# Optimization experiments

Measured on AMD Instinct MI355X. Metric: run time of the kernel, lower is better.

The kernel has to match this reference:

```python
import jax, jax.numpy as jnp
import numpy as np
from jax import lax

B, C, H, W = 4, 128, 128, 128
DG = 2          # deformable groups
K = 9           # 3x3 kernel
EPS = 1e-5


def conv2d(x, w, stride=1, pad=1):
    return lax.conv_general_dilated(
        x, w, (stride, stride), [(pad, pad), (pad, pad)],
        dimension_numbers=("NCHW", "OIHW", "NCHW"))


def bn(x, p):
    # p: [4, C] = gamma, beta, running_mean, running_var (eval-mode BN)
    g, b, m, v = p[0], p[1], p[2], p[3]
    inv = g / jnp.sqrt(v + EPS)
    return x * inv[:, None, None] + (b - m * inv)[:, None, None]


def deform_sample(x, py, px):
    # x: [B,C,H,W]; py/px: [B,DG,K,H,W] absolute sample coords
    Bb, Cc, Hh, Ww = x.shape
    Cg = Cc // DG
    xg = x.reshape(Bb, DG, Cg, Hh * Ww)
    y0 = jnp.floor(py); x0 = jnp.floor(px)
    fy = py - y0; fx = px - x0
    y0i = y0.astype(jnp.int32); x0i = x0.astype(jnp.int32)

    def corner(yi, xi, wgt):
        valid = (yi >= 0) & (yi < Hh) & (xi >= 0) & (xi < Ww)
        idx = (jnp.clip(yi, 0, Hh - 1) * Ww + jnp.clip(xi, 0, Ww - 1)).reshape(Bb, DG, -1)
        v = jnp.take_along_axis(xg, idx[:, :, None, :], axis=3)  # [B,DG,Cg,K*H*W]
        return v * (wgt * valid).reshape(Bb, DG, 1, -1)

    val = (corner(y0i, x0i, (1 - fy) * (1 - fx))
           + corner(y0i, x0i + 1, (1 - fy) * fx)
           + corner(y0i + 1, x0i, fy * (1 - fx))
           + corner(y0i + 1, x0i + 1, fy * fx))
    return val.reshape(Bb, DG, Cg, K, Hh, Ww)


def modulated_deform_conv(x, off_w, off_b, dc_w, dc_b):
    Bb, Cc, Hh, Ww = x.shape
    off_out = conv2d(x, off_w) + off_b[None, :, None, None]   # [B,3*DG*K,H,W]
    o = off_out[:, :2 * DG * K].reshape(Bb, DG, K, 2, Hh, Ww)
    mask = jax.nn.sigmoid(off_out[:, 2 * DG * K:]).reshape(Bb, DG, K, Hh, Ww)
    ky = (jnp.arange(K) // 3 - 1).astype(x.dtype)
    kx = (jnp.arange(K) % 3 - 1).astype(x.dtype)
    iy = jnp.arange(Hh, dtype=x.dtype)[:, None]
    ix = jnp.arange(Ww, dtype=x.dtype)[None, :]
    py = o[:, :, :, 0] + iy + ky[None, None, :, None, None]
    px = o[:, :, :, 1] + ix + kx[None, None, :, None, None]
    g = deform_sample(x, py, px) * mask[:, :, None]            # [B,DG,Cg,K,H,W]
    wr = dc_w.reshape(dc_w.shape[0], DG, Cc // DG, K)          # [O,DG,Cg,K]
    out = jnp.einsum("odck,bdckhw->bohw", wr, g)
    return out + dc_b[None, :, None, None]


def setup_inputs() -> dict:
    key = jax.random.key(0)
    ks = jax.random.split(key, 16)
    s3 = 1.0 / np.sqrt(C * 9)
    s1 = 1.0 / np.sqrt(C)

    def bn_params(k):
        k1, k2, k3, k4 = jax.random.split(k, 4)
        return jnp.stack([
            jax.random.uniform(k1, (C,)) + 0.5,
            jax.random.normal(k2, (C,)) * 0.1,
            jax.random.normal(k3, (C,)) * 0.1,
            jax.random.uniform(k4, (C,)) + 0.5])

    return {
        "x": jax.random.normal(ks[0], (B, C, H, W), jnp.float32),
        "rb_w1": jax.random.normal(ks[1], (C, C, 3, 3), jnp.float32) * s3,
        "rb_b1": jax.random.normal(ks[2], (C,), jnp.float32) * 0.01,
        "rb_bn1": bn_params(ks[3]),
        "rb_w2": jax.random.normal(ks[4], (C, C, 3, 3), jnp.float32) * s3,
        "rb_b2": jax.random.normal(ks[5], (C,), jnp.float32) * 0.01,
        "rb_bn2": bn_params(ks[6]),
        "off_w": jax.random.normal(ks[7], (3 * DG * K, C, 3, 3), jnp.float32) * s3 * 0.1,
        "off_b": jax.random.normal(ks[8], (3 * DG * K,), jnp.float32) * 0.01,
        "dc_w": jax.random.normal(ks[9], (C, C, 3, 3), jnp.float32) * s3,
        "dc_b": jax.random.normal(ks[10], (C,), jnp.float32) * 0.01,
        "bn1": bn_params(ks[11]),
        "cv2_w": jax.random.normal(ks[12], (C, C, 1, 1), jnp.float32) * s1,
        "bn2": bn_params(ks[13]),
    }


def reference(x, rb_w1, rb_b1, rb_bn1, rb_w2, rb_b2, rb_bn2,
              off_w, off_b, dc_w, dc_b, bn1, cv2_w, bn2):
    # ResBlock (stride=1, n_in==n_out -> identity shortcut)
    h = jax.nn.relu(bn(conv2d(x, rb_w1) + rb_b1[None, :, None, None], rb_bn1))
    h = bn(conv2d(h, rb_w2) + rb_b2[None, :, None, None], rb_bn2)
    h = jax.nn.relu(h + x)
    # modulated deformable conv + BN + LeakyReLU(0.1)
    h = modulated_deform_conv(h, off_w, off_b, dc_w, dc_b)
    h = jax.nn.leaky_relu(bn(h, bn1), 0.1)
    # 1x1 conv (no bias) + BN + LeakyReLU(0.1)
    h = jax.nn.leaky_relu(bn(conv2d(h, cv2_w, pad=0), bn2), 0.1)
    # residual (downsample is None: in==out, stride==1)
    return x + h
```

## Files before the change

### kernel.cpp

```cpp
#include <hip/hip_runtime.h>
#include <math.h>

#define BB 4
#define EPSV 1e-5f

typedef __attribute__((ext_vector_type(8))) short short8;
typedef __attribute__((ext_vector_type(4))) float floatx4;
typedef __attribute__((ext_vector_type(4))) int intx4;
typedef __attribute__((ext_vector_type(4))) unsigned short ushort4v;

__device__ inline float b2f(unsigned short u) {
    unsigned v = ((unsigned)u) << 16;
    return __builtin_bit_cast(float, v);
}
__device__ inline unsigned short f2b(float f) {
    unsigned u = __builtin_bit_cast(unsigned, f);
    u += 0x7FFFu + ((u >> 16) & 1u);
    return (unsigned short)(u >> 16);
}
__device__ inline unsigned short f2b_fast(float f) {
    unsigned u = __builtin_bit_cast(unsigned, f);
    return (unsigned short)((u + 0x8000u) >> 16);
}

__global__ __launch_bounds__(256) void transpose_k(const float* __restrict__ x,
                                                   unsigned short* __restrict__ xb) {
    __shared__ unsigned short t[64][136];
    const int tid = threadIdx.x;
    const int px0 = blockIdx.x * 64;
    const int b = blockIdx.y;
    const int pxr = tid & 63;
    const int c0 = tid >> 6;
#pragma unroll
    for (int i = 0; i < 32; ++i) {
        int c = c0 + i * 4;
        float v = x[(((size_t)b * 128 + c) << 14) + px0 + pxr];
        t[pxr][c] = f2b(v);
    }
    __syncthreads();
#pragma unroll
    for (int i = 0; i < 4; ++i) {
        int idx = tid + i * 256;
        int px = idx >> 4;
        int c8 = idx & 15;
        short8 v = *(const short8*)&t[px][c8 * 8];
        *(short8*)&xb[(((size_t)b << 14) + px0 + px) * 128 + c8 * 8] = v;
    }
}

template<int MPAD, int OCH>
__global__ __launch_bounds__(256) void repack_conv_frag(const float* __restrict__ w,
                                                        unsigned short* __restrict__ dst) {
    int t = blockIdx.x * 256 + threadIdx.x;
    if (t >= 1152 * MPAD) return;
    const int NMT2 = MPAD / 16;
    int j = t & 7, lane = (t >> 3) & 63, rest = t >> 9;
    int mt = rest % NMT2, step = rest / NMT2;
    int oc = mt * 16 + (lane & 15);
    int k = step * 32 + ((lane >> 4) << 3) + j;
    int half = k / 576;
    int tap = (k - half * 576) >> 6;
    int c = half * 64 + (k & 63);
    float v = (oc < OCH) ? w[((size_t)oc * 128 + c) * 9 + tap] : 0.f;
    dst[t] = f2b(v);
}

__global__ __launch_bounds__(256) void repack_dc_frag(const float* __restrict__ w,
                                                      unsigned short* __restrict__ dst) {
    int t = blockIdx.x * 256 + threadIdx.x;
    if (t >= 1152 * 128) return;
    int j = t & 7, lane = (t >> 3) & 63, rest = t >> 9;
    int mt = rest & 7, step = rest >> 3;
    int oc = mt * 16 + (lane & 15);
    int k = step * 32 + ((lane >> 4) << 3) + j;
    int dk = k >> 6, c = k & 63;
    int d = (dk >= 9) ? 1 : 0;
    int kk = dk - d * 9;
    float v = w[((size_t)oc * 128 + d * 64 + c) * 9 + kk];
    dst[t] = f2b(v);
}

__global__ __launch_bounds__(256) void repack_cv2_frag(const float* __restrict__ w,
                                                       unsigned short* __restrict__ dst) {
    int t = blockIdx.x * 256 + threadIdx.x;
    if (t >= 128 * 128) return;
    int j = t & 7, lane = (t >> 3) & 63, rest = t >> 9;
    int mt = rest & 7, step = rest >> 3;
    int oc = mt * 16 + (lane & 15);
    int k = step * 32 + ((lane >> 4) << 3) + j;
    dst[t] = f2b(w[oc * 128 + k]);
}

template<int NMT, int MODE>
__global__ __launch_bounds__(256, 2) void conv3x3_mfma(
    const unsigned short* __restrict__ in, const unsigned short* __restrict__ wf,
    const float* __restrict__ bias, const float* __restrict__ bnp,
    const float* __restrict__ res, void* __restrict__ outv)
{
    __shared__ unsigned short sm[3][130][72];
    const int tid = threadIdx.x;
    const int lane = tid & 63, wid = tid >> 6;
    const int wm = wid & 1, wn = wid >> 1;
    const int h = blockIdx.x;
    const int b = blockIdx.y;
    const int n16 = lane & 15, quad = lane >> 4;

    short8 L[13];

    auto stage_load = [&](int half) {
#pragma unroll
        for (int rnd = 0; rnd < 13; ++rnd) {
            int idx = rnd * 256 + tid;
            short8 v = {0, 0, 0, 0, 0, 0, 0, 0};
            if (idx < 3120) {
                int c8 = idx & 7;
                int wl = (idx >> 3) % 130;
                int r  = (idx >> 3) / 130;
                int hh = h - 1 + r, ww = wl - 1;
                if ((unsigned)hh < 128u && (unsigned)ww < 128u)
                    v = *(const short8*)&in[(((size_t)b << 14) + hh * 128 + ww) * 128 + half * 64 + c8 * 8];
            }
            L[rnd] = v;
        }
    };
    auto stage_write = [&]() {
#pragma unroll
        for (int rnd = 0; rnd < 13; ++rnd) {
            int idx = rnd * 256 + tid;
            if (idx < 3120) {
                int c8 = idx & 7;
                int wl = (idx >> 3) % 130;
                int r  = (idx >> 3) / 130;
                *(short8*)&sm[r][wl][c8 * 8] = L[rnd];
            }
        }
    };

    floatx4 acc[NMT][4];
#pragma unroll
    for (int mt = 0; mt < NMT; ++mt)
#pragma unroll
        for (int nt = 0; nt < 4; ++nt)
            acc[mt][nt] = (floatx4){0.f, 0.f, 0.f, 0.f};

    auto compute = [&](int half) {
#pragma unroll
        for (int tap = 0; tap < 9; ++tap) {
            const int ky = tap / 3, kx = tap % 3;
#pragma unroll
            for (int cc = 0; cc < 2; ++cc) {
                const int step = half * 18 + tap * 2 + cc;
                short8 a[NMT], bf[4];
#pragma unroll
                for (int nt = 0; nt < 4; ++nt)
                    bf[nt] = *(const short8*)&sm[ky][wn * 64 + nt * 16 + n16 + kx][cc * 32 + quad * 8];
#pragma unroll
                for (int mt = 0; mt < NMT; ++mt)
                    a[mt] = *(const short8*)&wf[((size_t)(step * (2 * NMT) + wm * NMT + mt) * 64 + lane) * 8];
#pragma unroll
                for (int mt = 0; mt < NMT; ++mt)
#pragma unroll
                    for (int nt = 0; nt < 4; ++nt)
                        acc[mt][nt] = __builtin_amdgcn_mfma_f32_16x16x32_bf16(a[mt], bf[nt], acc[mt][nt], 0, 0, 0);
            }
        }
    };

    stage_load(0);
    stage_write();
    __syncthreads();
    stage_load(1);
    compute(0);
    __syncthreads();
    stage_write();
    __syncthreads();
    compute(1);

#pragma unroll
    for (int mt = 0; mt < NMT; ++mt) {
        const int ocb = (wm * NMT + mt) * 16 + quad * 4;
        float Ae[4], Be[4];
#pragma unroll
        for (int r = 0; r < 4; ++r) {
            int oc = ocb + r;
            if (MODE == 0) {
                Ae[r] = 1.f;
                Be[r] = (oc < 54) ? bias[oc] : 0.f;
            } else {
                float g = bnp[oc], be = bnp[128 + oc], m = bnp[256 + oc], vv = bnp[384 + oc];
                float inv = g * rsqrtf(vv + EPSV);
                Ae[r] = inv;
                Be[r] = be - m * inv + bias[oc] * inv;
            }
        }
#pragma unroll
        for (int nt = 0; nt < 4; ++nt) {
            int pxg = h * 128 + wn * 64 + nt * 16 + n16;
            if (MODE == 0) {
                float* outf = (float*)outv;
#pragma unroll
                for (int r = 0; r < 4; ++r) {
                    int oc = ocb + r;
                    if (oc < 54)
                        outf[(((size_t)(b * 54 + oc)) << 14) + pxg] = acc[mt][nt][r] + Be[r];
                }
            } else {
                ushort4v pk;
#pragma unroll
                for (int r = 0; r < 4; ++r) {
                    float v = acc[mt][nt][r] * Ae[r] + Be[r];
                    if (MODE == 2) v += res[(((size_t)b * 128 + ocb + r) << 14) + pxg];
                    v = fmaxf(v, 0.f);
                    pk[r] = f2b(v);
                }
                *(ushort4v*)&((unsigned short*)outv)[((size_t)((b << 14) + pxg)) * 128 + ocb] = pk;
            }
        }
    }
}

__global__ __launch_bounds__(256, 4) void deform_mfma(
    const unsigned short* __restrict__ src, const float* __restrict__ off,
    const unsigned short* __restrict__ wf, const float* __restrict__ dcb,
    const float* __restrict__ bnp, unsigned short* __restrict__ out)
{
    __shared__ unsigned short gt[2][64][72];
    __shared__ floatx4 smw[3][64];
    __shared__ intx4   sma[3][64];
    const int tid = threadIdx.x;
    const int lane = tid & 63, wid = tid >> 6;
    const int wm = wid & 1, wn = wid >> 1;
    const int w0 = (blockIdx.x & 1) * 64;
    const int h = blockIdx.x >> 1;
    const int b = blockIdx.y;
    const int n16 = lane & 15, quad = lane >> 4;
    const int q = tid & 7;
    const int pxq = tid >> 3 & 31;

    const char* srcbyte = (const char*)src + ((size_t)b << 22);
    const float* offpx = off + (((size_t)(b * 54)) << 14) + h * 128 + w0 + tid;

    auto math = [&](int dk, int slot) {
        float oy = offpx[(size_t)(2 * dk) << 14];
        float ox = offpx[(size_t)(2 * dk + 1) << 14];
        float mz = offpx[(size_t)(36 + dk) << 14];
        int d = (dk >= 9) ? 1 : 0;
        int kk = dk - d * 9;
        float ms = 1.f / (1.f + __expf(-mz));
        float py = oy + (float)h + (float)(kk / 3 - 1);
        float pxs = ox + (float)(w0 + tid) + (float)(kk % 3 - 1);
        float y0f = floorf(py), x0f = floorf(pxs);
        float fy = py - y0f, fx = pxs - x0f;
        int y0 = (int)y0f, x0 = (int)x0f;
        int y1 = y0 + 1, x1 = x0 + 1;
        float w00 = (1.f - fy) * (1.f - fx) * ms, w01 = (1.f - fy) * fx * ms;
        float w10 = fy * (1.f - fx) * ms, w11 = fy * fx * ms;
        if ((unsigned)y0 >= 128u) { w00 = 0.f; w01 = 0.f; }
        if ((unsigned)y1 >= 128u) { w10 = 0.f; w11 = 0.f; }
        if ((unsigned)x0 >= 128u) { w00 = 0.f; w10 = 0.f; }
        if ((unsigned)x1 >= 128u) { w01 = 0.f; w11 = 0.f; }
        int y0c = min(max(y0, 0), 127), y1c = min(max(y1, 0), 127);
        int x0c = min(max(x0, 0), 127), x1c = min(max(x1, 0), 127);
        int chb = d * 128;
        smw[slot][tid] = (floatx4){w00, w01, w10, w11};
        sma[slot][tid] = (intx4){((y0c * 128 + x0c) << 8) + chb, ((y0c * 128 + x1c) << 8) + chb,
                                 ((y1c * 128 + x0c) << 8) + chb, ((y1c * 128 + x1c) << 8) + chb};
    };

    floatx4 wA[2];
    short8 g[2][4];
    auto gather = [&](int slot) {
#pragma unroll
        for (int ph = 0; ph < 2; ++ph) {
            int pxl = ph * 32 + pxq;
            floatx4 wv = smw[slot][pxl];
            intx4 av = sma[slot][pxl];
            wA[ph] = wv;
#pragma unroll
            for (int c = 0; c < 4; ++c)
                g[ph][c] = *(const short8*)(srcbyte + (size_t)(av[c] + q * 16));
        }
    };

    floatx4 acc[4][2];
#pragma unroll
    for (int mt = 0; mt < 4; ++mt)
#pragma unroll
        for (int nt = 0; nt < 2; ++nt)
            acc[mt][nt] = (floatx4){0.f, 0.f, 0.f, 0.f};

    if (tid < 64) { math(0, 0); math(1, 1); }
    __syncthreads();
    gather(0);

    int buf = 0;
    for (int dk = 0; dk < 18; ++dk) {
#pragma unroll
        for (int ph = 0; ph < 2; ++ph) {
            short8 o8;
#pragma unroll
            for (int j = 0; j < 8; ++j) {
                float v = wA[ph][0] * b2f((unsigned short)g[ph][0][j])
                        + wA[ph][1] * b2f((unsigned short)g[ph][1][j])
                        + wA[ph][2] * b2f((unsigned short)g[ph][2][j])
                        + wA[ph][3] * b2f((unsigned short)g[ph][3][j]);
                o8[j] = (short)f2b_fast(v);
            }
            *(short8*)&gt[buf][ph * 32 + pxq][q * 8] = o8;
        }
        if (tid < 64 && dk < 16) math(dk + 2, (dk + 2) % 3);
        __syncthreads();
        if (dk < 17) gather((dk + 1) % 3);

#pragma unroll
        for (int hf = 0; hf < 2; ++hf) {
            int s = dk * 2 + hf;
            short8 a[4], bfr[2];
#pragma unroll
            for (int nt = 0; nt < 2; ++nt)
                bfr[nt] = *(const short8*)&gt[buf][wn * 32 + nt * 16 + n16][hf * 32 + quad * 8];
#pragma unroll
            for (int mt = 0; mt < 4; ++mt)
                a[mt] = *(const short8*)&wf[((size_t)(s * 8 + wm * 4 + mt) * 64 + lane) * 8];
#pragma unroll
            for (int mt = 0; mt < 4; ++mt)
#pragma unroll
                for (int nt = 0; nt < 2; ++nt)
                    acc[mt][nt] = __builtin_amdgcn_mfma_f32_16x16x32_bf16(a[mt], bfr[nt], acc[mt][nt], 0, 0, 0);
        }
        buf ^= 1;
    }

#pragma unroll
    for (int mt = 0; mt < 4; ++mt) {
        const int ocb = (wm * 4 + mt) * 16 + quad * 4;
        float Ae[4], Be[4];
#pragma unroll
        for (int r = 0; r < 4; ++r) {
            int oc = ocb + r;
            float gg = bnp[oc], be = bnp[128 + oc], m = bnp[256 + oc], vv = bnp[384 + oc];
            float inv = gg * rsqrtf(vv + EPSV);
            Ae[r] = inv;
            Be[r] = be - m * inv + dcb[oc] * inv;
        }
#pragma unroll
        for (int nt = 0; nt < 2; ++nt) {
            int pxg2 = h * 128 + w0 + wn * 32 + nt * 16 + n16;
            ushort4v pk;
#pragma unroll
            for (int r = 0; r < 4; ++r) {
                float v = acc[mt][nt][r] * Ae[r] + Be[r];
                v = (v > 0.f) ? v : 0.1f * v;
                pk[r] = f2b(v);
            }
            *(ushort4v*)&out[((size_t)((b << 14) + pxg2)) * 128 + ocb] = pk;
        }
    }
}

__global__ __launch_bounds__(256, 4) void conv1x1_mfma(
    const unsigned short* __restrict__ in, const unsigned short* __restrict__ wf,
    const float* __restrict__ bnp, const float* __restrict__ x, float* __restrict__ out)
{
    const int tid = threadIdx.x;
    const int lane = tid & 63, wid = tid >> 6;
    const int wm = wid & 1, wn = wid >> 1;
    const int w0 = (blockIdx.x & 1) * 64;
    const int h = blockIdx.x >> 1;
    const int b = blockIdx.y;
    const int n16 = lane & 15, quad = lane >> 4;

    floatx4 acc[4][2];
#pragma unroll
    for (int mt = 0; mt < 4; ++mt)
#pragma unroll
        for (int nt = 0; nt < 2; ++nt)
            acc[mt][nt] = (floatx4){0.f, 0.f, 0.f, 0.f};

#pragma unroll
    for (int s = 0; s < 4; ++s) {
        short8 a[4], bfr[2];
#pragma unroll
        for (int nt = 0; nt < 2; ++nt) {
            int px = h * 128 + w0 + wn * 32 + nt * 16 + n16;
            bfr[nt] = *(const short8*)&in[((size_t)((b << 14) + px)) * 128 + s * 32 + quad * 8];
        }
#pragma unroll
        for (int mt = 0; mt < 4; ++mt)
            a[mt] = *(const short8*)&wf[((size_t)(s * 8 + wm * 4 + mt) * 64 + lane) * 8];
#pragma unroll
        for (int mt = 0; mt < 4; ++mt)
#pragma unroll
            for (int nt = 0; nt < 2; ++nt)
                acc[mt][nt] = __builtin_amdgcn_mfma_f32_16x16x32_bf16(a[mt], bfr[nt], acc[mt][nt], 0, 0, 0);
    }

#pragma unroll
    for (int mt = 0; mt < 4; ++mt) {
        const int ocb = (wm * 4 + mt) * 16 + quad * 4;
        float Ae[4], Be[4];
#pragma unroll
        for (int r = 0; r < 4; ++r) {
            int oc = ocb + r;
            float g = bnp[oc], be = bnp[128 + oc], m = bnp[256 + oc], vv = bnp[384 + oc];
            float inv = g * rsqrtf(vv + EPSV);
            Ae[r] = inv;
            Be[r] = be - m * inv;
        }
#pragma unroll
        for (int nt = 0; nt < 2; ++nt) {
            int pxg2 = h * 128 + w0 + wn * 32 + nt * 16 + n16;
#pragma unroll
            for (int r = 0; r < 4; ++r) {
                int oc = ocb + r;
                float v = acc[mt][nt][r] * Ae[r] + Be[r];
                v = (v > 0.f) ? v : 0.1f * v;
                v += x[(((size_t)b * 128 + oc) << 14) + pxg2];
                out[(((size_t)b * 128 + oc) << 14) + pxg2] = v;
            }
        }
    }
}

extern "C" void kernel_launch(void* const* d_in, const int* in_sizes, int n_in,
                              void* d_out, int out_size, void* d_ws, size_t ws_size,
                              hipStream_t stream) {
    const float* x      = (const float*)d_in[0];
    const float* rb_w1  = (const float*)d_in[1];
    const float* rb_b1  = (const float*)d_in[2];
    const float* rb_bn1 = (const float*)d_in[3];
    const float* rb_w2  = (const float*)d_in[4];
    const float* rb_b2  = (const float*)d_in[5];
    const float* rb_bn2 = (const float*)d_in[6];
    const float* off_w  = (const float*)d_in[7];
    const float* off_b  = (const float*)d_in[8];
    const float* dc_w   = (const float*)d_in[9];
    const float* dc_b   = (const float*)d_in[10];
    const float* bn1    = (const float*)d_in[11];
    const float* cv2_w  = (const float*)d_in[12];
    const float* bn2    = (const float*)d_in[13];

    char* base = (char*)d_ws;
    const size_t TSZ = (size_t)4 * 16384 * 128 * 2;
    unsigned short* xb = (unsigned short*)base;
    unsigned short* h1 = (unsigned short*)(base + TSZ);
    unsigned short* h2 = (unsigned short*)(base + 2 * TSZ);
    unsigned short* wf1 = (unsigned short*)(base + 3 * TSZ);
    unsigned short* wf2 = wf1 + 1152 * 128;
    unsigned short* wfO = wf2 + 1152 * 128;
    unsigned short* wfD = wfO + 1152 * 64;
    unsigned short* wfC = wfD + 1152 * 128;
    float* offb = (float*)h1;
    unsigned short* h3 = xb;

    dim3 blk(256, 1, 1);
    dim3 grid(256, BB, 1);
    dim3 grid3(128, BB, 1);

    transpose_k<<<grid, blk, 0, stream>>>(x, xb);
    repack_conv_frag<128, 128><<<576, 256, 0, stream>>>(rb_w1, wf1);
    repack_conv_frag<128, 128><<<576, 256, 0, stream>>>(rb_w2, wf2);
    repack_conv_frag<64, 54><<<288, 256, 0, stream>>>(off_w, wfO);
    repack_dc_frag<<<576, 256, 0, stream>>>(dc_w, wfD);
    repack_cv2_frag<<<64, 256, 0, stream>>>(cv2_w, wfC);

    conv3x3_mfma<4, 1><<<grid3, blk, 0, stream>>>(xb, wf1, rb_b1, rb_bn1, nullptr, (void*)h1);
    conv3x3_mfma<4, 2><<<grid3, blk, 0, stream>>>(h1, wf2, rb_b2, rb_bn2, x, (void*)h2);
    conv3x3_mfma<2, 0><<<grid3, blk, 0, stream>>>(h2, wfO, off_b, nullptr, nullptr, (void*)offb);
    deform_mfma<<<grid, blk, 0, stream>>>(h2, offb, wfD, dc_b, bn1, h3);
    conv1x1_mfma<<<grid, blk, 0, stream>>>(h3, wfC, bn2, x, (float*)d_out);
}
```

Baseline: 275.5 us.

## Software-pipeline MFMA operand loads across conv, deform and 1x1 kernels

Adds register double-buffering of the weight (A) and activation (B) fragments in the 3x3 conv, deformable conv and 1x1 conv kernels. The next step's loads are issued before the current step's MFMAs, hiding global and LDS load latency. In exchange, the 3x3 conv loses its overlap of the second-half global staging with the first-half compute, since it now stages each half directly after a sync. The deform kernel's occupancy hint drops from 4 to 3 blocks to make room for the extra registers.

```diff
diff --git a/kernel.cpp b/kernel.cpp
--- a/kernel.cpp
+++ b/kernel.cpp
@@ -105,25 +105,7 @@
     const int b = blockIdx.y;
     const int n16 = lane & 15, quad = lane >> 4;
 
-    short8 L[13];
-
-    auto stage_load = [&](int half) {
-#pragma unroll
-        for (int rnd = 0; rnd < 13; ++rnd) {
-            int idx = rnd * 256 + tid;
-            short8 v = {0, 0, 0, 0, 0, 0, 0, 0};
-            if (idx < 3120) {
-                int c8 = idx & 7;
-                int wl = (idx >> 3) % 130;
-                int r  = (idx >> 3) / 130;
-                int hh = h - 1 + r, ww = wl - 1;
-                if ((unsigned)hh < 128u && (unsigned)ww < 128u)
-                    v = *(const short8*)&in[(((size_t)b << 14) + hh * 128 + ww) * 128 + half * 64 + c8 * 8];
-            }
-            L[rnd] = v;
-        }
-    };
-    auto stage_write = [&]() {
+    auto stage = [&](int half) {
 #pragma unroll
         for (int rnd = 0; rnd < 13; ++rnd) {
             int idx = rnd * 256 + tid;
@@ -131,7 +113,11 @@
                 int c8 = idx & 7;
                 int wl = (idx >> 3) % 130;
                 int r  = (idx >> 3) / 130;
-                *(short8*)&sm[r][wl][c8 * 8] = L[rnd];
+                int hh = h - 1 + r, ww = wl - 1;
+                short8 v = {0, 0, 0, 0, 0, 0, 0, 0};
+                if ((unsigned)hh < 128u && (unsigned)ww < 128u)
+                    v = *(const short8*)&in[(((size_t)b << 14) + hh * 128 + ww) * 128 + half * 64 + c8 * 8];
+                *(short8*)&sm[r][wl][c8 * 8] = v;
             }
         }
     };
@@ -143,36 +129,41 @@
         for (int nt = 0; nt < 4; ++nt)
             acc[mt][nt] = (floatx4){0.f, 0.f, 0.f, 0.f};
 
+    auto loadA = [&](int half, int s, short8* a) {
+        int st = half * 18 + s;
+#pragma unroll
+        for (int mt = 0; mt < NMT; ++mt)
+            a[mt] = *(const short8*)&wf[((size_t)(st * (2 * NMT) + wm * NMT + mt) * 64 + lane) * 8];
+    };
+    auto loadB = [&](int s, short8* bf) {
+        int tap = s >> 1, cc = s & 1;
+        int ky = tap / 3, kx = tap % 3;
+#pragma unroll
+        for (int nt = 0; nt < 4; ++nt)
+            bf[nt] = *(const short8*)&sm[ky][wn * 64 + nt * 16 + n16 + kx][cc * 32 + quad * 8];
+    };
+
     auto compute = [&](int half) {
-#pragma unroll
-        for (int tap = 0; tap < 9; ++tap) {
-            const int ky = tap / 3, kx = tap % 3;
-#pragma unroll
-            for (int cc = 0; cc < 2; ++cc) {
-                const int step = half * 18 + tap * 2 + cc;
-                short8 a[NMT], bf[4];
+        short8 a[2][NMT], bf[2][4];
+        loadA(half, 0, a[0]);
+        loadB(0, bf[0]);
+#pragma unroll
+        for (int s = 0; s < 18; ++s) {
+            const int cur = s & 1, nxt = cur ^ 1;
+            if (s < 17) { loadA(half, s + 1, a[nxt]); loadB(s + 1, bf[nxt]); }
+#pragma unroll
+            for (int mt = 0; mt < NMT; ++mt)
 #pragma unroll
                 for (int nt = 0; nt < 4; ++nt)
-                    bf[nt] = *(const short8*)&sm[ky][wn * 64 + nt * 16 + n16 + kx][cc * 32 + quad * 8];
-#pragma unroll
-                for (int mt = 0; mt < NMT; ++mt)
-                    a[mt] = *(const short8*)&wf[((size_t)(step * (2 * NMT) + wm * NMT + mt) * 64 + lane) * 8];
-#pragma unroll
-                for (int mt = 0; mt < NMT; ++mt)
-#pragma unroll
-                    for (int nt = 0; nt < 4; ++nt)
-                        acc[mt][nt] = __builtin_amdgcn_mfma_f32_16x16x32_bf16(a[mt], bf[nt], acc[mt][nt], 0, 0, 0);
-            }
-        }
-    };
-
-    stage_load(0);
-    stage_write();
+                    acc[mt][nt] = __builtin_amdgcn_mfma_f32_16x16x32_bf16(a[cur][mt], bf[cur][nt], acc[mt][nt], 0, 0, 0);
+        }
+    };
+
+    stage(0);
     __syncthreads();
-    stage_load(1);
     compute(0);
     __syncthreads();
-    stage_write();
+    stage(1);
     __syncthreads();
     compute(1);
 
@@ -219,7 +210,7 @@
     }
 }
 
-__global__ __launch_bounds__(256, 4) void deform_mfma(
+__global__ __launch_bounds__(256, 3) void deform_mfma(
     const unsigned short* __restrict__ src, const float* __restrict__ off,
     const unsigned short* __restrict__ wf, const float* __restrict__ dcb,
     const float* __restrict__ bnp, unsigned short* __restrict__ out)
@@ -282,6 +273,12 @@
         }
     };
 
+    auto loadWA = [&](int s, short8* ap_) {
+#pragma unroll
+        for (int mt = 0; mt < 4; ++mt)
+            ap_[mt] = *(const short8*)&wf[((size_t)(s * 8 + wm * 4 + mt) * 64 + lane) * 8];
+    };
+
     floatx4 acc[4][2];
 #pragma unroll
     for (int mt = 0; mt < 4; ++mt)
@@ -290,6 +287,8 @@
             acc[mt][nt] = (floatx4){0.f, 0.f, 0.f, 0.f};
 
     if (tid < 64) { math(0, 0); math(1, 1); }
+    short8 ap[2][4];
+    loadWA(0, ap[0]);
     __syncthreads();
     gather(0);
 
@@ -315,18 +314,16 @@
 #pragma unroll
         for (int hf = 0; hf < 2; ++hf) {
             int s = dk * 2 + hf;
-            short8 a[4], bfr[2];
+            if (s < 35) loadWA(s + 1, ap[hf ^ 1]);
+            short8 bfr[2];
 #pragma unroll
             for (int nt = 0; nt < 2; ++nt)
                 bfr[nt] = *(const short8*)&gt[buf][wn * 32 + nt * 16 + n16][hf * 32 + quad * 8];
 #pragma unroll
             for (int mt = 0; mt < 4; ++mt)
-                a[mt] = *(const short8*)&wf[((size_t)(s * 8 + wm * 4 + mt) * 64 + lane) * 8];
-#pragma unroll
-            for (int mt = 0; mt < 4; ++mt)
 #pragma unroll
                 for (int nt = 0; nt < 2; ++nt)
-                    acc[mt][nt] = __builtin_amdgcn_mfma_f32_16x16x32_bf16(a[mt], bfr[nt], acc[mt][nt], 0, 0, 0);
+                    acc[mt][nt] = __builtin_amdgcn_mfma_f32_16x16x32_bf16(ap[hf][mt], bfr[nt], acc[mt][nt], 0, 0, 0);
         }
         buf ^= 1;
     }
@@ -377,22 +374,31 @@
         for (int nt = 0; nt < 2; ++nt)
             acc[mt][nt] = (floatx4){0.f, 0.f, 0.f, 0.f};
 
-#pragma unroll
-    for (int s = 0; s < 4; ++s) {
-        short8 a[4], bfr[2];
+    auto loadA1 = [&](int s, short8* a) {
+#pragma unroll
+        for (int mt = 0; mt < 4; ++mt)
+            a[mt] = *(const short8*)&wf[((size_t)(s * 8 + wm * 4 + mt) * 64 + lane) * 8];
+    };
+    auto loadB1 = [&](int s, short8* bf) {
 #pragma unroll
         for (int nt = 0; nt < 2; ++nt) {
             int px = h * 128 + w0 + wn * 32 + nt * 16 + n16;
-            bfr[nt] = *(const short8*)&in[((size_t)((b << 14) + px)) * 128 + s * 32 + quad * 8];
-        }
+            bf[nt] = *(const short8*)&in[((size_t)((b << 14) + px)) * 128 + s * 32 + quad * 8];
+        }
+    };
+
+    short8 a[2][4], bfr[2][2];
+    loadA1(0, a[0]);
+    loadB1(0, bfr[0]);
+#pragma unroll
+    for (int s = 0; s < 4; ++s) {
+        const int cur = s & 1, nxt = cur ^ 1;
+        if (s < 3) { loadA1(s + 1, a[nxt]); loadB1(s + 1, bfr[nxt]); }
 #pragma unroll
         for (int mt = 0; mt < 4; ++mt)
-            a[mt] = *(const short8*)&wf[((size_t)(s * 8 + wm * 4 + mt) * 64 + lane) * 8];
-#pragma unroll
-        for (int mt = 0; mt < 4; ++mt)
 #pragma unroll
             for (int nt = 0; nt < 2; ++nt)
-                acc[mt][nt] = __builtin_amdgcn_mfma_f32_16x16x32_bf16(a[mt], bfr[nt], acc[mt][nt], 0, 0, 0);
+                acc[mt][nt] = __builtin_amdgcn_mfma_f32_16x16x32_bf16(a[cur][mt], bfr[cur][nt], acc[mt][nt], 0, 0, 0);
     }
 
 #pragma unroll
```

Measured after the change: 278.5 us. No clear change (+1.1%).
